# Performance work log

Measured on AMD Instinct MI355X. Metric: run time of the kernel, lower is better.

Reference implementation:

```python
import jax, jax.numpy as jnp
import numpy as np

TAU_S = 5.0  # network_config['tau_s']; n_steps inferred from trailing dim


def psp(x, tau_s):
    """Leaky synaptic integrator along the last (time) axis.
    x: [B, C, H, W, T] -> syns: [B, C, H, W, T]
    syn_t = syn_{t-1} * (1 - 1/tau_s) + x_t ;  out_t = syn_t / tau_s
    """
    decay = 1.0 - 1.0 / tau_s
    xt = jnp.moveaxis(x, -1, 0)  # [T, B, C, H, W]

    def step(syn, inp):
        syn = syn * decay + inp
        return syn, syn / tau_s

    _, ys = jax.lax.scan(step, jnp.zeros_like(xt[0]), xt)
    return jnp.moveaxis(ys, 0, -1)  # [B, C, H, W, T]


def setup_inputs() -> dict:
    key = jax.random.key(0)
    k1, k2 = jax.random.split(key)
    B, C, H, W, T = 32, 256, 4, 4, 100
    outputs = jax.random.normal(k1, (B, C, H, W, T), dtype=jnp.float32)
    # target is a spike train in the original; uniform [0,1) floats keep the
    # same math and dtype (fill='rand' per input_specs)
    target = jax.random.uniform(k2, (B, C, H, W, T), dtype=jnp.float32)
    return {"outputs": outputs, "target": target}


def reference(outputs, target):
    # spike_kernel: delta = outputs - psp(target); loss = 0.5 * sum(delta^2)
    delta = outputs - psp(target, TAU_S)
    return 0.5 * jnp.sum(delta * delta)
```

## Files before the change

### kernel.cpp

```cpp
#include <hip/hip_runtime.h>


#define BLOCK 1024
#define WPB   (BLOCK / 64)
#define GTILE 4
#define TILES 65536

constexpr double dpow(double b, int n) {
  double r = 1.0; for (int i = 0; i < n; ++i) r *= b; return r;
}
constexpr float K1  = (float)dpow(0.4096, 1);
constexpr float K2  = (float)dpow(0.4096, 2);
constexpr float K4  = (float)dpow(0.4096, 4);
constexpr float K8  = (float)dpow(0.4096, 8);
constexpr float K16 = (float)dpow(0.4096, 16);
constexpr float B0 = (float)(0.2 * dpow(0.8, 1));
constexpr float B1 = (float)(0.2 * dpow(0.8, 2));
constexpr float B2 = (float)(0.2 * dpow(0.8, 3));
constexpr float B3 = (float)(0.2 * dpow(0.8, 4));
constexpr float G4C = (float)(0.04 * (dpow(0.8, 2) + dpow(0.8, 4) +
                                      dpow(0.8, 6) + dpow(0.8, 8)));

__global__ __launch_bounds__(BLOCK) void spike_loss_kernel(
    const float4* __restrict__ o4g, const float4* __restrict__ x4g,
    float* __restrict__ out) {
  const int t    = threadIdx.x;
  const int lane = t & 63;
  const int w    = t >> 6;
  const int W    = blockIdx.x * WPB + w;
  const bool active = lane < 50;
  const int lidx = active ? lane : 49;
  const int seg  = (lidx < 25) ? lidx : lidx - 25;

  const size_t f4base = (size_t)W * (GTILE * 50) + lidx;
  const float4* op = o4g + f4base;
  const float4* xp = x4g + f4base;

  float4 ov[GTILE], xv[GTILE];
#pragma unroll
  for (int g = 0; g < GTILE; ++g) { ov[g] = op[g * 50]; xv[g] = xp[g * 50]; }

  float loss = 0.f;
#pragma unroll
  for (int g = 0; g < GTILE; ++g) {
    float u, a, abar, bbar;
    u = xv[g].x;                 a = fmaf(-0.2f, u, ov[g].x);
    abar = a * a;                bbar = a * B0;
    u = fmaf(0.8f, u, xv[g].y);  a = fmaf(-0.2f, u, ov[g].y);
    abar = fmaf(a, a, abar);     bbar = fmaf(a, B1, bbar);
    u = fmaf(0.8f, u, xv[g].z);  a = fmaf(-0.2f, u, ov[g].z);
    abar = fmaf(a, a, abar);     bbar = fmaf(a, B2, bbar);
    u = fmaf(0.8f, u, xv[g].w);  a = fmaf(-0.2f, u, ov[g].w);
    abar = fmaf(a, a, abar);     bbar = fmaf(a, B3, bbar);

    float c = u, up;
    up = __shfl_up(c, 1, 64);  if (seg >= 1)  c = fmaf(K1,  up, c);
    up = __shfl_up(c, 2, 64);  if (seg >= 2)  c = fmaf(K2,  up, c);
    up = __shfl_up(c, 4, 64);  if (seg >= 4)  c = fmaf(K4,  up, c);
    up = __shfl_up(c, 8, 64);  if (seg >= 8)  c = fmaf(K8,  up, c);
    up = __shfl_up(c, 16, 64); if (seg >= 16) c = fmaf(K16, up, c);
    up = __shfl_up(c, 1, 64);
    float sigma = (seg > 0) ? up : 0.f;

    float contrib = fmaf(G4C * sigma - 2.f * bbar, sigma, abar);
    loss += active ? contrib : 0.f;
  }

#pragma unroll
  for (int off = 32; off > 0; off >>= 1) loss += __shfl_down(loss, off, 64);

  __shared__ float wsum[WPB];
  if (lane == 0) wsum[w] = loss;
  __syncthreads();
  if (t < 64) {
    float v = (t < WPB) ? wsum[t] : 0.f;
#pragma unroll
    for (int off = 8; off > 0; off >>= 1) v += __shfl_down(v, off, 64);
    if (t == 0) atomicAdd(out, 0.5f * v);
  }
}

extern "C" void kernel_launch(void* const* d_in, const int* in_sizes, int n_in,
                              void* d_out, int out_size, void* d_ws, size_t ws_size,
                              hipStream_t stream) {
  const float4* o4 = (const float4*)d_in[0];
  const float4* x4 = (const float4*)d_in[1];
  float* loss = (float*)d_out;

  const int tiles = in_sizes[0] / 200;
  const int grid  = tiles / (WPB * GTILE);

  hipLaunchKernelGGL(spike_loss_kernel, dim3(grid), dim3(BLOCK), 0, stream,
                     o4, x4, loss);
}
```

Baseline: 116.8 us.

## Assign one time row per thread with sequential scan and register prefetch

Replaces the warp-cooperative parallel-prefix scan, where each lane held 4 timesteps and combined across lanes with shuffles, with a plain per-thread sequential recurrence over the full 100-step row. Loads are double-buffered in chunks of five float4s to overlap memory with compute, and the block size drops from 1024 to 256. This removes the shuffles, the idle lanes (only 50 of 64 were active) and the closed-form correction terms. In exchange, each thread's loads are now strided by 400 bytes across lanes, so global accesses are no longer coalesced, which may hurt a kernel that is mostly memory-bound.

```diff
diff --git a/kernel.cpp b/kernel.cpp
--- a/kernel.cpp
+++ b/kernel.cpp
@@ -1,82 +1,56 @@
 #include <hip/hip_runtime.h>
 
 
-#define BLOCK 1024
-#define WPB   (BLOCK / 64)
-#define GTILE 4
-#define TILES 65536
-
-constexpr double dpow(double b, int n) {
-  double r = 1.0; for (int i = 0; i < n; ++i) r *= b; return r;
-}
-constexpr float K1  = (float)dpow(0.4096, 1);
-constexpr float K2  = (float)dpow(0.4096, 2);
-constexpr float K4  = (float)dpow(0.4096, 4);
-constexpr float K8  = (float)dpow(0.4096, 8);
-constexpr float K16 = (float)dpow(0.4096, 16);
-constexpr float B0 = (float)(0.2 * dpow(0.8, 1));
-constexpr float B1 = (float)(0.2 * dpow(0.8, 2));
-constexpr float B2 = (float)(0.2 * dpow(0.8, 3));
-constexpr float B3 = (float)(0.2 * dpow(0.8, 4));
-constexpr float G4C = (float)(0.04 * (dpow(0.8, 2) + dpow(0.8, 4) +
-                                      dpow(0.8, 6) + dpow(0.8, 8)));
+#define BLOCK 256
 
 __global__ __launch_bounds__(BLOCK) void spike_loss_kernel(
     const float4* __restrict__ o4g, const float4* __restrict__ x4g,
     float* __restrict__ out) {
-  const int t    = threadIdx.x;
-  const int lane = t & 63;
-  const int w    = t >> 6;
-  const int W    = blockIdx.x * WPB + w;
-  const bool active = lane < 50;
-  const int lidx = active ? lane : 49;
-  const int seg  = (lidx < 25) ? lidx : lidx - 25;
+  const int r = blockIdx.x * BLOCK + threadIdx.x;
+  const float4* __restrict__ op = o4g + (size_t)r * 25;
+  const float4* __restrict__ xp = x4g + (size_t)r * 25;
 
-  const size_t f4base = (size_t)W * (GTILE * 50) + lidx;
-  const float4* op = o4g + f4base;
-  const float4* xp = x4g + f4base;
+  float4 xc[5], oc[5], xn[5], on[5];
+#pragma unroll
+  for (int j = 0; j < 5; ++j) { xc[j] = xp[j]; oc[j] = op[j]; }
 
-  float4 ov[GTILE], xv[GTILE];
+  float syn = 0.f;
+  float l0 = 0.f, l1 = 0.f, l2 = 0.f, l3 = 0.f;
 #pragma unroll
-  for (int g = 0; g < GTILE; ++g) { ov[g] = op[g * 50]; xv[g] = xp[g * 50]; }
-
-  float loss = 0.f;
+  for (int c = 0; c < 5; ++c) {
+    if (c < 4) {
 #pragma unroll
-  for (int g = 0; g < GTILE; ++g) {
-    float u, a, abar, bbar;
-    u = xv[g].x;                 a = fmaf(-0.2f, u, ov[g].x);
-    abar = a * a;                bbar = a * B0;
-    u = fmaf(0.8f, u, xv[g].y);  a = fmaf(-0.2f, u, ov[g].y);
-    abar = fmaf(a, a, abar);     bbar = fmaf(a, B1, bbar);
-    u = fmaf(0.8f, u, xv[g].z);  a = fmaf(-0.2f, u, ov[g].z);
-    abar = fmaf(a, a, abar);     bbar = fmaf(a, B2, bbar);
-    u = fmaf(0.8f, u, xv[g].w);  a = fmaf(-0.2f, u, ov[g].w);
-    abar = fmaf(a, a, abar);     bbar = fmaf(a, B3, bbar);
-
-    float c = u, up;
-    up = __shfl_up(c, 1, 64);  if (seg >= 1)  c = fmaf(K1,  up, c);
-    up = __shfl_up(c, 2, 64);  if (seg >= 2)  c = fmaf(K2,  up, c);
-    up = __shfl_up(c, 4, 64);  if (seg >= 4)  c = fmaf(K4,  up, c);
-    up = __shfl_up(c, 8, 64);  if (seg >= 8)  c = fmaf(K8,  up, c);
-    up = __shfl_up(c, 16, 64); if (seg >= 16) c = fmaf(K16, up, c);
-    up = __shfl_up(c, 1, 64);
-    float sigma = (seg > 0) ? up : 0.f;
-
-    float contrib = fmaf(G4C * sigma - 2.f * bbar, sigma, abar);
-    loss += active ? contrib : 0.f;
+      for (int j = 0; j < 5; ++j) {
+        xn[j] = xp[(c + 1) * 5 + j];
+        on[j] = op[(c + 1) * 5 + j];
+      }
+    }
+#pragma unroll
+    for (int j = 0; j < 5; ++j) {
+      float a;
+      syn = fmaf(0.8f, syn, xc[j].x); a = fmaf(-0.2f, syn, oc[j].x); l0 = fmaf(a, a, l0);
+      syn = fmaf(0.8f, syn, xc[j].y); a = fmaf(-0.2f, syn, oc[j].y); l1 = fmaf(a, a, l1);
+      syn = fmaf(0.8f, syn, xc[j].z); a = fmaf(-0.2f, syn, oc[j].z); l2 = fmaf(a, a, l2);
+      syn = fmaf(0.8f, syn, xc[j].w); a = fmaf(-0.2f, syn, oc[j].w); l3 = fmaf(a, a, l3);
+    }
+    if (c < 4) {
+#pragma unroll
+      for (int j = 0; j < 5; ++j) { xc[j] = xn[j]; oc[j] = on[j]; }
+    }
   }
+  float loss = (l0 + l1) + (l2 + l3);
 
 #pragma unroll
   for (int off = 32; off > 0; off >>= 1) loss += __shfl_down(loss, off, 64);
 
-  __shared__ float wsum[WPB];
+  __shared__ float wsum[BLOCK / 64];
+  const int lane = threadIdx.x & 63;
+  const int w    = threadIdx.x >> 6;
   if (lane == 0) wsum[w] = loss;
   __syncthreads();
-  if (t < 64) {
-    float v = (t < WPB) ? wsum[t] : 0.f;
-#pragma unroll
-    for (int off = 8; off > 0; off >>= 1) v += __shfl_down(v, off, 64);
-    if (t == 0) atomicAdd(out, 0.5f * v);
+  if (threadIdx.x == 0) {
+    float v = (wsum[0] + wsum[1]) + (wsum[2] + wsum[3]);
+    atomicAdd(out, 0.5f * v);
   }
 }
 
@@ -87,8 +61,8 @@
   const float4* x4 = (const float4*)d_in[1];
   float* loss = (float*)d_out;
 
-  const int tiles = in_sizes[0] / 200;
-  const int grid  = tiles / (WPB * GTILE);
+  const int rows = in_sizes[0] / 100;
+  const int grid = rows / BLOCK;
 
   hipLaunchKernelGGL(spike_loss_kernel, dim3(grid), dim3(BLOCK), 0, stream,
                      o4, x4, loss);
```

After: 143.2 us. 1.23x slower.

## Use all 64 lanes with cross-segment carry instead of idle-lane 50-wide tiles

Applied to the files above, without the earlier changes.

Each wave now covers contiguous runs of 64 float4 elements (8 groups) rather than 50-lane tiles, so no lanes sit idle. Time series of 25 float4 chunks now straddle lane and group boundaries. This is handled by carrying the running synaptic state across groups, weighting it with exp2-based decay powers, and recomputing the incoming carry from the preceding chunk at the start of each wave. The block size drops to 256 and the final reduction becomes four scalar adds. The extra shuffles, the exp2f call and the carry bookkeeping add latency and arithmetic, and accumulating through the carry may change floating-point rounding slightly.

```diff
diff --git a/kernel.cpp b/kernel.cpp
--- a/kernel.cpp
+++ b/kernel.cpp
@@ -1,10 +1,9 @@
 #include <hip/hip_runtime.h>
 
 
-#define BLOCK 1024
+#define BLOCK 256
 #define WPB   (BLOCK / 64)
-#define GTILE 4
-#define TILES 65536
+#define G     8
 
 constexpr double dpow(double b, int n) {
   double r = 1.0; for (int i = 0; i < n; ++i) r *= b; return r;
@@ -20,6 +19,7 @@
 constexpr float B3 = (float)(0.2 * dpow(0.8, 4));
 constexpr float G4C = (float)(0.04 * (dpow(0.8, 2) + dpow(0.8, 4) +
                                       dpow(0.8, 6) + dpow(0.8, 8)));
+constexpr float L2D4 = -1.2877123795494493f;
 
 __global__ __launch_bounds__(BLOCK) void spike_loss_kernel(
     const float4* __restrict__ o4g, const float4* __restrict__ x4g,
@@ -28,21 +28,37 @@
   const int lane = t & 63;
   const int w    = t >> 6;
   const int W    = blockIdx.x * WPB + w;
-  const bool active = lane < 50;
-  const int lidx = active ? lane : 49;
-  const int seg  = (lidx < 25) ? lidx : lidx - 25;
+  const size_t gs = (size_t)W * (G * 64);
+  const int b    = (int)(gs % 25);
 
-  const size_t f4base = (size_t)W * (GTILE * 50) + lidx;
-  const float4* op = o4g + f4base;
-  const float4* xp = x4g + f4base;
+  const float Wl = exp2f((float)(lane + 1) * L2D4);
+  int p = b + lane;
+  p -= (p >= 75) ? 75 : (p >= 50) ? 50 : (p >= 25) ? 25 : 0;
 
-  float4 ov[GTILE], xv[GTILE];
+  const float4* op = o4g + gs + lane;
+  const float4* xp = x4g + gs + lane;
+
+  float4 ov[G], xv[G];
 #pragma unroll
-  for (int g = 0; g < GTILE; ++g) { ov[g] = op[g * 50]; xv[g] = xp[g * 50]; }
+  for (int g = 0; g < G; ++g) { ov[g] = op[g * 64]; xv[g] = xp[g * 64]; }
+
+  float C = 0.f;
+  if (b) {
+    float pu = 0.f;
+    if (lane < b) {
+      float4 px = x4g[gs - b + lane];
+      float u = px.x;
+      u = fmaf(0.8f, u, px.y); u = fmaf(0.8f, u, px.z); u = fmaf(0.8f, u, px.w);
+      pu = u * exp2f((float)(b - 1 - lane) * L2D4);
+    }
+#pragma unroll
+    for (int off = 32; off; off >>= 1) pu += __shfl_xor(pu, off, 64);
+    C = pu;
+  }
 
   float loss = 0.f;
 #pragma unroll
-  for (int g = 0; g < GTILE; ++g) {
+  for (int g = 0; g < G; ++g) {
     float u, a, abar, bbar;
     u = xv[g].x;                 a = fmaf(-0.2f, u, ov[g].x);
     abar = a * a;                bbar = a * B0;
@@ -53,17 +69,22 @@
     u = fmaf(0.8f, u, xv[g].w);  a = fmaf(-0.2f, u, ov[g].w);
     abar = fmaf(a, a, abar);     bbar = fmaf(a, B3, bbar);
 
+    const int q = min(p, lane);
     float c = u, up;
-    up = __shfl_up(c, 1, 64);  if (seg >= 1)  c = fmaf(K1,  up, c);
-    up = __shfl_up(c, 2, 64);  if (seg >= 2)  c = fmaf(K2,  up, c);
-    up = __shfl_up(c, 4, 64);  if (seg >= 4)  c = fmaf(K4,  up, c);
-    up = __shfl_up(c, 8, 64);  if (seg >= 8)  c = fmaf(K8,  up, c);
-    up = __shfl_up(c, 16, 64); if (seg >= 16) c = fmaf(K16, up, c);
+    up = __shfl_up(c, 1, 64);  if (q >= 1)  c = fmaf(K1,  up, c);
+    up = __shfl_up(c, 2, 64);  if (q >= 2)  c = fmaf(K2,  up, c);
+    up = __shfl_up(c, 4, 64);  if (q >= 4)  c = fmaf(K4,  up, c);
+    up = __shfl_up(c, 8, 64);  if (q >= 8)  c = fmaf(K8,  up, c);
+    up = __shfl_up(c, 16, 64); if (q >= 16) c = fmaf(K16, up, c);
+    if (p > lane) c = fmaf(Wl, C, c);
+    float Cn = __shfl(c, 63, 64);
     up = __shfl_up(c, 1, 64);
-    float sigma = (seg > 0) ? up : 0.f;
+    float sigma = (p > 0) ? (lane ? up : C) : 0.f;
 
-    float contrib = fmaf(G4C * sigma - 2.f * bbar, sigma, abar);
-    loss += active ? contrib : 0.f;
+    loss += fmaf(fmaf(G4C, sigma, -2.f * bbar), sigma, abar);
+
+    C = Cn;
+    p += 14; if (p >= 25) p -= 25;
   }
 
 #pragma unroll
@@ -72,11 +93,9 @@
   __shared__ float wsum[WPB];
   if (lane == 0) wsum[w] = loss;
   __syncthreads();
-  if (t < 64) {
-    float v = (t < WPB) ? wsum[t] : 0.f;
-#pragma unroll
-    for (int off = 8; off > 0; off >>= 1) v += __shfl_down(v, off, 64);
-    if (t == 0) atomicAdd(out, 0.5f * v);
+  if (t == 0) {
+    float v = (wsum[0] + wsum[1]) + (wsum[2] + wsum[3]);
+    atomicAdd(out, 0.5f * v);
   }
 }
 
@@ -87,8 +106,7 @@
   const float4* x4 = (const float4*)d_in[1];
   float* loss = (float*)d_out;
 
-  const int tiles = in_sizes[0] / 200;
-  const int grid  = tiles / (WPB * GTILE);
+  const int grid = in_sizes[0] / (8 * 64 * 4 * WPB);
 
   hipLaunchKernelGGL(spike_loss_kernel, dim3(grid), dim3(BLOCK), 0, stream,
                      o4, x4, loss);
```

After: 124.2 us. 1.06x slower.
